# Kernel optimization log

Hardware: AMD Instinct MI355X
Metric: run time of the kernel (lower is better)

Reference implementation:

```python
import jax, jax.numpy as jnp
import numpy as np

B, S, E, H, WIN = 1, 2048, 1024, 16, 256
D = E // H  # head_out = 64


def setup_inputs() -> dict:
    key = jax.random.key(0)
    ks = jax.random.split(key, 10)
    w = lambda k: jax.random.normal(k, (E, E), jnp.float32) * 0.02
    return {
        'x': jax.random.normal(ks[0], (B, S, E), jnp.float32),
        'global_attention_mask': jax.random.randint(ks[1], (B, S), 0, 2).astype(jnp.int32),
        'W_local_query': w(ks[2]),
        'W_local_key': w(ks[3]),
        'W_local_value': w(ks[4]),
        'W_query': w(ks[5]),
        'W_key': w(ks[6]),
        'W_value': w(ks[7]),
        'W_proj': w(ks[8]),
        'b_proj': jnp.zeros((E,), jnp.float32),
    }


def reference(x, global_attention_mask, W_local_query, W_local_key, W_local_value,
              W_query, W_key, W_value, W_proj, b_proj):
    b, seq, emb = x.shape
    nH, dh, win = H, D, WIN
    chunks = seq // win
    NEG = -1e9
    scale = 1.0 / (dh ** 0.5)

    # ---- local (windowed) branch ----
    ql = x @ W_local_query            # [b,S,E]
    kl = x @ W_local_key
    vl = x @ W_local_value
    # NOTE: original does a direct .view -> plain reshape (no head transpose)
    qc = ql.reshape(b, nH, chunks, win, dh)
    kc = kl.reshape(b, nH, chunks, win, dh)
    vloc = vl.reshape(b, nH, seq, dh)
    s = jnp.einsum('bhcqd,bhckd->bhcqk', qc, kc)      # [b,H,C,W,W]
    causal_w = jnp.tril(jnp.ones((win, win), bool))
    s = jnp.where(causal_w, s, NEG) * scale           # mask then /sqrt(d), as in source
    s = s.mean(axis=2)                                # mean over chunks -> [b,H,W,W]
    s = jnp.pad(s, ((0, 0), (0, 0), (0, seq - win), (0, seq - win)))
    aw_l = jax.nn.softmax(s, axis=-1)                 # [b,H,S,S]
    local_ctx = jnp.einsum('bhqk,bhkd->bqhd', aw_l, vloc).reshape(b, seq, emb)

    # ---- global (full) branch ----
    q = (x @ W_query).reshape(b, seq, nH, dh).transpose(0, 2, 1, 3)
    k = (x @ W_key).reshape(b, seq, nH, dh).transpose(0, 2, 1, 3)
    v = (x @ W_value).reshape(b, seq, nH, dh).transpose(0, 2, 1, 3)
    sg = jnp.einsum('bhqd,bhkd->bhqk', q, k)          # [b,H,S,S]
    causal_s = jnp.tril(jnp.ones((seq, seq), bool))
    sg = jnp.where(causal_s, sg, NEG) * scale
    aw_g = jax.nn.softmax(sg, axis=-1)
    gctx = jnp.einsum('bhqk,bhkd->bqhd', aw_g, v).reshape(b, seq, emb)

    # ---- combine via global mask, then output projection ----
    ctx = jnp.where(global_attention_mask[:, :, None] == 1, gctx, local_ctx)
    return ctx @ W_proj + b_proj
```

## Files before the change

kernel.cpp:

```cpp
#include <hip/hip_runtime.h>
#include <hip/hip_bf16.h>

typedef _Float16 h8 __attribute__((ext_vector_type(8)));
typedef _Float16 h4 __attribute__((ext_vector_type(4)));
typedef _Float16 h2 __attribute__((ext_vector_type(2)));
typedef __fp16 fp16x2 __attribute__((ext_vector_type(2)));
typedef float f4 __attribute__((ext_vector_type(4)));

#define S_LEN 2048
#define EMB 1024
#define NH 16
#define DH 64

__device__ __forceinline__ void async_copy16(const void* g, void* l) {
  __builtin_amdgcn_global_load_lds(
      (const __attribute__((address_space(1))) void*)g,
      (__attribute__((address_space(3))) void*)l, 16, 0, 0);
}

__device__ __forceinline__ f4 mfma16(h8 a, h8 b, f4 c) {
  return __builtin_amdgcn_mfma_f32_16x16x32_f16(a, b, c, 0, 0, 0);
}

__device__ __forceinline__ h2 cvt_pk(float a, float b) {
  const fp16x2 r = __builtin_amdgcn_cvt_pkrtz(a, b);
  return __builtin_bit_cast(h2, r);
}

__global__ __launch_bounds__(256) void prep_kernel(
    const float* __restrict__ x, const float* w0, const float* w1, const float* w2,
    const float* w3, const float* w4, const float* w5, const float* w6,
    _Float16* __restrict__ xh, _Float16* __restrict__ Wtb) {
  const int bid = blockIdx.x;
  if (bid < 2048) {
    const int i = bid * 256 + threadIdx.x;
    const float4 v = *(const float4*)&x[(long)i * 4];
    h4 o;
    o.x = (_Float16)v.x; o.y = (_Float16)v.y; o.z = (_Float16)v.z; o.w = (_Float16)v.w;
    *(h4*)&xh[(long)i * 4] = o;
    return;
  }
  const int b2 = bid - 2048;
  const int z = b2 >> 10, rem = b2 & 1023;
  const float* W = w0;
  switch (z) {
    case 1: W = w1; break; case 2: W = w2; break; case 3: W = w3; break;
    case 4: W = w4; break; case 5: W = w5; break; case 6: W = w6; break;
    default: break;
  }
  __shared__ float t[32][33];
  const int bk = (rem & 31) * 32, bn = (rem >> 5) * 32;
  const int tx = threadIdx.x & 31, ty = threadIdx.x >> 5;
  #pragma unroll
  for (int i = 0; i < 4; ++i)
    t[ty + i * 8][tx] = W[(long)(bk + ty + i * 8) * 1024 + bn + tx];
  __syncthreads();
  _Float16* o = Wtb + (long)z * 1048576;
  #pragma unroll
  for (int i = 0; i < 4; ++i)
    o[(long)(bn + ty + i * 8) * 1024 + bk + tx] = (_Float16)t[tx][ty + i * 8];
}

__global__ __launch_bounds__(256) void shuffle_kernel(
    const _Float16* __restrict__ ql, const _Float16* __restrict__ kl,
    const _Float16* __restrict__ vl, const _Float16* __restrict__ vg,
    const int* __restrict__ gmask,
    _Float16* __restrict__ Aq, _Float16* __restrict__ Ak,
    _Float16* __restrict__ vgT, float* __restrict__ Vall, float* __restrict__ Vtail,
    int* __restrict__ qsel, int* __restrict__ qcnt) {
  const int bid = blockIdx.x;
  if (bid < 2048) {
    const _Float16* src = (bid >= 1024) ? kl : ql;
    _Float16* dst = (bid >= 1024) ? Ak : Aq;
    const int u = (bid & 1023) * 256 + threadIdx.x;
    const int dseg = u & 7, c = (u >> 3) & 7, q = (u >> 6) & 255, h = u >> 14;
    const long soff = (long)(h * 128 + c * 16 + (q >> 4)) * 1024 + (q & 15) * 64 + dseg * 8;
    *(h8*)&dst[(long)u * 8] = *(const h8*)&src[soff];
    return;
  }
  if (bid < 4096) {
    const int b2 = bid - 2048;
    __shared__ _Float16 t[32][33];
    const int bs = (b2 & 63) * 32, be = (b2 >> 6) * 32;
    const int tx = threadIdx.x & 31, ty = threadIdx.x >> 5;
    #pragma unroll
    for (int i = 0; i < 4; ++i)
      t[ty + i * 8][tx] = vg[(long)(bs + ty + i * 8) * 1024 + be + tx];
    __syncthreads();
    #pragma unroll
    for (int i = 0; i < 4; ++i)
      vgT[(long)(be + ty + i * 8) * 2048 + bs + tx] = t[tx][ty + i * 8];
    return;
  }
  if (bid < 4112) {
    const int hh = bid - 4096;
    const int d = threadIdx.x & 63, g = threadIdx.x >> 6;
    float sall = 0.f, shead = 0.f;
    for (int i = 0; i < 32; ++i) {
      const int ro = g * 32 + i;
      const _Float16* base = vl + (long)(hh * 128 + ro) * 1024 + d;
      #pragma unroll
      for (int j = 0; j < 16; ++j) {
        const float v = (float)base[j * 64];
        sall += v;
        if (ro < 16) shead += v;
      }
    }
    __shared__ float sA[4][64], sH[4][64];
    sA[g][d] = sall; sH[g][d] = shead;
    __syncthreads();
    if (g == 0) {
      const float a = sA[0][d] + sA[1][d] + sA[2][d] + sA[3][d];
      const float hsum = sH[0][d] + sH[1][d] + sH[2][d] + sH[3][d];
      Vall[hh * 64 + d] = a;
      Vtail[hh * 64 + d] = a - hsum;
    }
    return;
  }
  const int t = threadIdx.x;
  int m8[8], cnt8 = 0;
  #pragma unroll
  for (int j = 0; j < 8; ++j) {
    m8[j] = gmask[t * 8 + j];
    cnt8 += (m8[j] == 1);
  }
  __shared__ int sc[256];
  sc[t] = cnt8;
  __syncthreads();
  for (int off = 1; off < 256; off <<= 1) {
    const int v = (t >= off) ? sc[t - off] : 0;
    __syncthreads();
    sc[t] += v;
    __syncthreads();
  }
  int base = sc[t] - cnt8;
  #pragma unroll
  for (int j = 0; j < 8; ++j)
    if (m8[j] == 1) qsel[base++] = t * 8 + j;
  if (t == 255) qcnt[0] = sc[255];
}

__global__ __launch_bounds__(512, 2) void gemm256_kernel(
    const _Float16* __restrict__ A, const _Float16* __restrict__ Bt,
    _Float16* __restrict__ C) {
  const int bid = blockIdx.x;
  const int bxx = (bid >> 3) & 7;
  const int byy = (bid & 7) * 3 + (bid >> 6);
  const int bm = bxx * 256, bn = byy * 256;

  __shared__ alignas(16) _Float16 As[2][2][8192];
  __shared__ alignas(16) _Float16 Bs[2][2][8192];

  const int tid = threadIdx.x;
  const int w = tid >> 6, l = tid & 63;
  const int lo = l & 15, hi = l >> 4;
  const int wm = w >> 2, wn = w & 3;
  const int srow = tid >> 3;
  const int kseg = (tid & 7) ^ (srow & 7);

  const _Float16* Bb = Bt + (long)(byy >> 2) * 1048576 + (long)(bn & 1023) * 1024;

#define STG_A(db, half, tt) do {                                                     \
    const int t_ = (tt) < 15 ? (tt) : 15;                                            \
    const _Float16* s_ = A + (long)(bm + (half) * 128 + srow) * 1024 + t_ * 64 + kseg * 8; \
    async_copy16(s_, &As[db][half][w * 512]);                                        \
    async_copy16(s_ + 65536, &As[db][half][4096 + w * 512]);                         \
  } while (0)
#define STG_B(db, half, tt) do {                                                     \
    const int t_ = (tt) < 15 ? (tt) : 15;                                            \
    const _Float16* s_ = Bb + (long)((half) * 128 + srow) * 1024 + t_ * 64 + kseg * 8; \
    async_copy16(s_, &Bs[db][half][w * 512]);                                        \
    async_copy16(s_ + 65536, &Bs[db][half][4096 + w * 512]);                         \
  } while (0)
#define LDA(db, mg) do { _Pragma("unroll")                                           \
    for (int fr = 0; fr < 4; ++fr) {                                                 \
      const int rr = wm * 64 + fr * 16 + lo;                                         \
      _Pragma("unroll") for (int kk = 0; kk < 2; ++kk)                               \
        af[fr][kk] = *(const h8*)&As[db][mg][rr * 64 + (((kk * 4 + hi) ^ (rr & 7)) * 8)]; \
    } } while (0)
#define LDB(db, ng) do { _Pragma("unroll")                                           \
    for (int fc = 0; fc < 2; ++fc) {                                                 \
      const int rr = wn * 32 + fc * 16 + lo;                                         \
      _Pragma("unroll") for (int kk = 0; kk < 2; ++kk)                               \
        bf[ng][fc][kk] = *(const h8*)&Bs[db][ng][rr * 64 + (((kk * 4 + hi) ^ (rr & 7)) * 8)]; \
    } } while (0)
#define MFMA_PH(mg, ng) do {                                                         \
    __builtin_amdgcn_s_setprio(1);                                                   \
    _Pragma("unroll") for (int fr = 0; fr < 4; ++fr)                                 \
      _Pragma("unroll") for (int fc = 0; fc < 2; ++fc) {                             \
        acc[mg][fr][ng][fc] = mfma16(af[fr][0], bf[ng][fc][0], acc[mg][fr][ng][fc]); \
        acc[mg][fr][ng][fc] = mfma16(af[fr][1], bf[ng][fc][1], acc[mg][fr][ng][fc]); \
      }                                                                              \
    __builtin_amdgcn_s_setprio(0);                                                   \
  } while (0)
#define BARR do { asm volatile("" ::: "memory"); __builtin_amdgcn_s_barrier();       \
                  asm volatile("" ::: "memory"); } while (0)
#define VM8 asm volatile("s_waitcnt vmcnt(8)" ::: "memory")

  const f4 zero = {0.f, 0.f, 0.f, 0.f};
  f4 acc[2][4][2][2];
  #pragma unroll
  for (int a_ = 0; a_ < 2; ++a_)
    #pragma unroll
    for (int b_ = 0; b_ < 4; ++b_)
      #pragma unroll
      for (int c_ = 0; c_ < 2; ++c_)
        #pragma unroll
        for (int d_ = 0; d_ < 2; ++d_) acc[a_][b_][c_][d_] = zero;
  h8 af[4][2];
  h8 bf[2][2][2];

  STG_A(0, 0, 0); STG_B(0, 0, 0); STG_A(0, 1, 0); STG_B(0, 1, 0);
  STG_A(1, 0, 1); STG_B(1, 0, 1); STG_A(1, 1, 1);
  asm volatile("s_waitcnt vmcnt(6)" ::: "memory");
  BARR;

  for (int i = 0; i < 8; ++i) {
    const int t2 = 2 * i + 2, t3 = 2 * i + 3;
    LDA(0, 0); LDB(0, 0); STG_B(1, 1, 2 * i + 1); MFMA_PH(0, 0); VM8; BARR;
    LDB(0, 1); STG_A(0, 0, t2); MFMA_PH(0, 1); BARR;
    LDA(0, 1); STG_B(0, 0, t2); MFMA_PH(1, 0); BARR;
    STG_A(0, 1, t2); MFMA_PH(1, 1); VM8; BARR;
    LDA(1, 0); LDB(1, 0); STG_B(0, 1, t2); MFMA_PH(0, 0); VM8; BARR;
    LDB(1, 1); STG_A(1, 0, t3); MFMA_PH(0, 1); BARR;
    LDA(1, 1); STG_B(1, 0, t3); MFMA_PH(1, 0); BARR;
    STG_A(1, 1, t3); MFMA_PH(1, 1); VM8; BARR;
  }

  #pragma unroll
  for (int mg = 0; mg < 2; ++mg)
    #pragma unroll
    for (int fr = 0; fr < 4; ++fr) {
      const int row = bm + mg * 128 + wm * 64 + fr * 16 + hi * 4;
      #pragma unroll
      for (int ng = 0; ng < 2; ++ng)
        #pragma unroll
        for (int fc = 0; fc < 2; ++fc) {
          const int colg = bn + ng * 128 + wn * 32 + fc * 16 + lo;
          _Float16* cp = C + (long)(colg >> 10) * 2097152 + (long)row * 1024 + (colg & 1023);
          #pragma unroll
          for (int r = 0; r < 4; ++r)
            cp[(long)r * 1024] = (_Float16)acc[mg][fr][ng][fc][r];
        }
    }
#undef STG_A
#undef STG_B
#undef LDA
#undef LDB
#undef MFMA_PH
#undef BARR
#undef VM8
}

template <bool F32OUT, bool HAS_BIAS>
__global__ __launch_bounds__(256) void gemm_kernel(
    const _Float16* __restrict__ A, const _Float16* __restrict__ Bt,
    void* __restrict__ Cv, const float* __restrict__ bias,
    int M, int N, int K, long sA, long sB, long sC) {
  const int bxx = blockIdx.x, byy = blockIdx.y, bzz = blockIdx.z;
  const _Float16* Ab = A + (long)bzz * sA;
  const _Float16* Bb = Bt + (long)bzz * sB;
  const int bm = bxx * 128, bn = byy * 128;
  __shared__ alignas(16) _Float16 As[128 * 64];
  __shared__ alignas(16) _Float16 Bs[128 * 64];
  const int tid = threadIdx.x;
  const int w = tid >> 6, l = tid & 63;
  const int lo = l & 15, hi = l >> 4;
  const int wr = (w >> 1) * 64, wc = (w & 1) * 64;
  const int srow = l >> 3, ssp = l & 7;
  const int ssl = ssp ^ (srow & 7);

  const f4 zero = {0.f, 0.f, 0.f, 0.f};
  f4 acc[4][4];
  #pragma unroll
  for (int m = 0; m < 4; ++m)
    #pragma unroll
    for (int n = 0; n < 4; ++n) acc[m][n] = zero;

  for (int k0 = 0; k0 < K; k0 += 64) {
    #pragma unroll
    for (int i = 0; i < 4; ++i) {
      const int chunk = w + i * 4;
      async_copy16(&Ab[(long)(bm + chunk * 8 + srow) * K + k0 + ssl * 8], &As[chunk * 512]);
      async_copy16(&Bb[(long)(bn + chunk * 8 + srow) * K + k0 + ssl * 8], &Bs[chunk * 512]);
    }
    __syncthreads();
    #pragma unroll
    for (int kk = 0; kk < 2; ++kk) {
      h8 af[4], bff[4];
      #pragma unroll
      for (int m = 0; m < 4; ++m) {
        const int r = wr + m * 16 + lo;
        af[m] = *(const h8*)&As[r * 64 + (((kk * 4 + hi) ^ (r & 7)) * 8)];
      }
      #pragma unroll
      for (int n = 0; n < 4; ++n) {
        const int r = wc + n * 16 + lo;
        bff[n] = *(const h8*)&Bs[r * 64 + (((kk * 4 + hi) ^ (r & 7)) * 8)];
      }
      #pragma unroll
      for (int m = 0; m < 4; ++m)
        #pragma unroll
        for (int n = 0; n < 4; ++n)
          acc[m][n] = mfma16(af[m], bff[n], acc[m][n]);
    }
    __syncthreads();
  }

  #pragma unroll
  for (int m = 0; m < 4; ++m) {
    const int row0 = bm + wr + m * 16 + hi * 4;
    #pragma unroll
    for (int n = 0; n < 4; ++n) {
      const int col = bn + wc + n * 16 + lo;
      float bv = 0.f;
      if constexpr (HAS_BIAS) bv = bias[col];
      #pragma unroll
      for (int r = 0; r < 4; ++r) {
        const float v = acc[m][n][r] + bv;
        const long off = (long)bzz * sC + (long)(row0 + r) * N + col;
        if constexpr (F32OUT) ((float*)Cv)[off] = v;
        else ((_Float16*)Cv)[off] = (_Float16)v;
      }
    }
  }
}

__global__ __launch_bounds__(256) void gemm64_kernel(
    const _Float16* __restrict__ A, const _Float16* __restrict__ Bt,
    float* __restrict__ C, const float* __restrict__ bias, int N, int K) {
  const int bm = blockIdx.x * 64, bn = blockIdx.y * 128;
  __shared__ alignas(16) _Float16 As[64 * 64];
  __shared__ alignas(16) _Float16 Bs[128 * 64];
  const int tid = threadIdx.x;
  const int w = tid >> 6, l = tid & 63;
  const int lo = l & 15, hi = l >> 4;
  const int wc = w * 32;
  const int srow = l >> 3, ssp = l & 7;
  const int ssl = ssp ^ (srow & 7);

  const f4 zero = {0.f, 0.f, 0.f, 0.f};
  f4 acc[4][2];
  #pragma unroll
  for (int m = 0; m < 4; ++m)
    #pragma unroll
    for (int n = 0; n < 2; ++n) acc[m][n] = zero;

  for (int k0 = 0; k0 < K; k0 += 64) {
    #pragma unroll
    for (int i = 0; i < 6; ++i) {
      const int c = w + i * 4;
      if (c < 8)
        async_copy16(&A[(long)(bm + c * 8 + srow) * K + k0 + ssl * 8], &As[c * 512]);
      else
        async_copy16(&Bt[(long)(bn + (c - 8) * 8 + srow) * K + k0 + ssl * 8], &Bs[(c - 8) * 512]);
    }
    __syncthreads();
    #pragma unroll
    for (int kk = 0; kk < 2; ++kk) {
      h8 af[4], bff[2];
      #pragma unroll
      for (int m = 0; m < 4; ++m) {
        const int r = m * 16 + lo;
        af[m] = *(const h8*)&As[r * 64 + (((kk * 4 + hi) ^ (r & 7)) * 8)];
      }
      #pragma unroll
      for (int n = 0; n < 2; ++n) {
        const int r = wc + n * 16 + lo;
        bff[n] = *(const h8*)&Bs[r * 64 + (((kk * 4 + hi) ^ (r & 7)) * 8)];
      }
      #pragma unroll
      for (int m = 0; m < 4; ++m)
        #pragma unroll
        for (int n = 0; n < 2; ++n)
          acc[m][n] = mfma16(af[m], bff[n], acc[m][n]);
    }
    __syncthreads();
  }

  #pragma unroll
  for (int m = 0; m < 4; ++m) {
    const int row0 = bm + m * 16 + hi * 4;
    #pragma unroll
    for (int n = 0; n < 2; ++n) {
      const int col = bn + wc + n * 16 + lo;
      const float bv = bias ? bias[col] : 0.f;
      #pragma unroll
      for (int r = 0; r < 4; ++r)
        C[(long)(row0 + r) * N + col] = acc[m][n][r] + bv;
    }
  }
}

__global__ __launch_bounds__(256) void flash_kernel(
    const _Float16* __restrict__ Q, const _Float16* __restrict__ Km,
    const _Float16* __restrict__ Vt, const int* __restrict__ qsel,
    const int* __restrict__ qcnt, _Float16* __restrict__ ctx,
    _Float16* __restrict__ pO, float2* __restrict__ ml) {
  const int bx = blockIdx.x;
  const int h = bx & 15;
  const int v = bx >> 4;
  const int tile = 31 - (v >> 1);
  const int chunk = v & 1;
  int cnt = qcnt[0];
  cnt = cnt < 1 ? 1 : (cnt > 2048 ? 2048 : cnt);
  if (tile * 64 >= cnt) return;
  const int L = (qsel[min(tile * 64 + 63, cnt - 1)] & 2047) + 1;
  const int ntot = (L + 63) >> 6;
  const bool chunked = (ntot > 16);
  if (!chunked && chunk) return;
  const int nsplit = chunked ? ((ntot + 1) >> 1) : ntot;
  const int t0 = chunk ? nsplit : 0;
  const int t1 = chunk ? ntot : nsplit;

  const int tid = threadIdx.x;
  const int w = tid >> 6, l = tid & 63;
  const int lo = l & 15, hi = l >> 4;
  const int row = tile * 64 + w * 16 + lo;
  const int qg = qsel[min(row, cnt - 1)] & 2047;

  __shared__ alignas(16) _Float16 Ks[2][64 * 64];
  __shared__ alignas(16) _Float16 Vs[2][64 * 64];
  __shared__ alignas(16) _Float16 Ps[4][16 * 80];
  _Float16* ps = Ps[w];

  const int rl = tid >> 3;
  const int ssl = (tid & 7) ^ (rl & 7);

#define STAGE(b, t)                                                                   \
  do {                                                                                \
    async_copy16(&Km[(long)((t) * 64 + rl) * EMB + h * DH + ssl * 8],                 \
                 &Ks[(b)][(w * 8) * 64]);                                             \
    async_copy16(&Km[(long)((t) * 64 + 32 + rl) * EMB + h * DH + ssl * 8],            \
                 &Ks[(b)][(w * 8 + 32) * 64]);                                        \
    async_copy16(&Vt[(long)(h * DH + rl) * S_LEN + (t) * 64 + ssl * 8],               \
                 &Vs[(b)][(w * 8) * 64]);                                             \
    async_copy16(&Vt[(long)(h * DH + 32 + rl) * S_LEN + (t) * 64 + ssl * 8],          \
                 &Vs[(b)][(w * 8 + 32) * 64]);                                        \
  } while (0)

  h8 qf[2];
  #pragma unroll
  for (int kk = 0; kk < 2; ++kk)
    qf[kk] = *(const h8*)&Q[(long)qg * EMB + h * DH + kk * 32 + hi * 8];

  const f4 zero = {0.f, 0.f, 0.f, 0.f};
  f4 o[4];
  #pragma unroll
  for (int nd = 0; nd < 4; ++nd) o[nd] = zero;
  float mr = -1e30f, lr = 0.f;
  const float SC = 0.125f * 1.44269504f;

  STAGE(0, t0);
  __syncthreads();
  int cur = 0;

  for (int t = t0; t < t1; ++t) {
    if (t + 1 < t1) STAGE(cur ^ 1, t + 1);

    const _Float16* ks = Ks[cur];
    const _Float16* vs = Vs[cur];

    __builtin_amdgcn_s_setprio(1);
    f4 s[4];
    #pragma unroll
    for (int n = 0; n < 4; ++n) {
      s[n] = zero;
      #pragma unroll
      for (int kk = 0; kk < 2; ++kk) {
        const int r = n * 16 + lo;
        const h8 kf = *(const h8*)&ks[r * 64 + (((kk * 4 + hi) ^ (lo & 7)) * 8)];
        s[n] = mfma16(kf, qf[kk], s[n]);
      }
    }
    __builtin_amdgcn_s_setprio(0);

    float sv[16];
    float tm = -1e30f;
    #pragma unroll
    for (int n = 0; n < 4; ++n)
      #pragma unroll
      for (int r = 0; r < 4; ++r) {
        float vv = s[n][r] * SC;
        if ((t * 64 + n * 16 + hi * 4 + r) > qg) vv = -1e30f;
        sv[n * 4 + r] = vv;
        tm = fmaxf(tm, vv);
      }
    tm = fmaxf(tm, __shfl_xor(tm, 16));
    tm = fmaxf(tm, __shfl_xor(tm, 32));
    const float mn = fmaxf(mr, tm);
    const float c = exp2f(mr - mn);
    mr = mn;
    float psum = 0.f;
    #pragma unroll
    for (int i = 0; i < 16; ++i) {
      sv[i] = exp2f(sv[i] - mr);
      psum += sv[i];
    }
    psum += __shfl_xor(psum, 16);
    psum += __shfl_xor(psum, 32);
    lr = lr * c + psum;

    #pragma unroll
    for (int n = 0; n < 4; ++n) {
      const int seg = (2 * n + (hi >> 1)) ^ (lo & 7);
      const int base = lo * 80 + seg * 8 + (hi & 1) * 4;
      *(h2*)&ps[base] = cvt_pk(sv[n * 4 + 0], sv[n * 4 + 1]);
      *(h2*)&ps[base + 2] = cvt_pk(sv[n * 4 + 2], sv[n * 4 + 3]);
    }
    h8 pb[2];
    #pragma unroll
    for (int kk = 0; kk < 2; ++kk)
      pb[kk] = *(const h8*)&ps[lo * 80 + (((kk * 4 + hi) ^ (lo & 7)) * 8)];

    __builtin_amdgcn_s_setprio(1);
    #pragma unroll
    for (int nd = 0; nd < 4; ++nd) {
      #pragma unroll
      for (int r = 0; r < 4; ++r) o[nd][r] *= c;
      #pragma unroll
      for (int kk = 0; kk < 2; ++kk) {
        const int rr = nd * 16 + lo;
        const h8 vf = *(const h8*)&vs[rr * 64 + (((kk * 4 + hi) ^ (lo & 7)) * 8)];
        o[nd] = mfma16(vf, pb[kk], o[nd]);
      }
    }
    __builtin_amdgcn_s_setprio(0);

    __syncthreads();
    cur ^= 1;
  }
#undef STAGE

  if (chunked) {
    const int slot = (h * 32 + tile) * 2 + chunk;
    _Float16* po = pO + (long)slot * 4096 + (w * 16 + lo) * 64;
    #pragma unroll
    for (int nd = 0; nd < 4; ++nd) {
      const h2 a = cvt_pk(o[nd][0], o[nd][1]);
      const h2 b = cvt_pk(o[nd][2], o[nd][3]);
      const h4 v4 = {a[0], a[1], b[0], b[1]};
      *(h4*)&po[nd * 16 + hi * 4] = v4;
    }
    if (hi == 0) ml[slot * 64 + w * 16 + lo] = make_float2(mr, lr);
  } else if (row < cnt) {
    const float inv = 1.f / lr;
    #pragma unroll
    for (int nd = 0; nd < 4; ++nd) {
      const h2 a = cvt_pk(o[nd][0] * inv, o[nd][1] * inv);
      const h2 b = cvt_pk(o[nd][2] * inv, o[nd][3] * inv);
      const h4 v4 = {a[0], a[1], b[0], b[1]};
      *(h4*)&ctx[(long)qg * EMB + h * DH + nd * 16 + hi * 4] = v4;
    }
  }
}

__global__ __launch_bounds__(256) void localfin_kernel(
    const _Float16* __restrict__ P, const _Float16* __restrict__ vl,
    const float* __restrict__ Vall, const float* __restrict__ Vtail,
    const _Float16* __restrict__ pO, const float2* __restrict__ ml,
    const int* __restrict__ gmask, const int* __restrict__ qsel,
    const int* __restrict__ qcnt, _Float16* __restrict__ ctx) {
  const int bid = blockIdx.x;
  const int tid = threadIdx.x;
  if (bid < 1024) {
    const int q = bid & 255, hg = bid >> 8;
    if (gmask[q] == 1) return;
    const int sub = tid >> 6, l = tid & 63;
    const int hh = hg * 4 + sub;
    __shared__ float wgt[4][256];
    const _Float16* Pr = P + ((long)hh * 256 + q) * 256;
    float sv[4];
    bool valid[4];
    float M = -1e30f;
    #pragma unroll
    for (int i = 0; i < 4; ++i) {
      const int k = l + i * 64;
      valid[i] = (k <= q);
      sv[i] = valid[i] ? (float)Pr[k] * 0.015625f : -1e30f;
      M = fmaxf(M, sv[i]);
    }
    M = fmaxf(M, __shfl_xor(M, 1));
    M = fmaxf(M, __shfl_xor(M, 2));
    M = fmaxf(M, __shfl_xor(M, 4));
    M = fmaxf(M, __shfl_xor(M, 8));
    M = fmaxf(M, __shfl_xor(M, 16));
    M = fmaxf(M, __shfl_xor(M, 32));
    M = fmaxf(M, 0.f);
    float ps = 0.f;
    #pragma unroll
    for (int i = 0; i < 4; ++i) {
      const float e = valid[i] ? __expf(sv[i] - M) : 0.f;
      wgt[sub][l + i * 64] = e;
      ps += e;
    }
    ps += __shfl_xor(ps, 1);
    ps += __shfl_xor(ps, 2);
    ps += __shfl_xor(ps, 4);
    ps += __shfl_xor(ps, 8);
    ps += __shfl_xor(ps, 16);
    ps += __shfl_xor(ps, 32);
    const float em = __expf(-M);
    const float denom = ps + 1792.f * em;
    const int d = l;
    float acc = em * Vtail[hh * 64 + d];
    const _Float16* vb = vl + (long)hh * 128 * 1024 + d;
    for (int k = 0; k <= q; ++k)
      acc += wgt[sub][k] * (float)vb[(long)(k >> 4) * 1024 + (k & 15) * 64];
    ctx[(long)q * EMB + hh * DH + d] = (_Float16)(acc / denom);
    return;
  }
  if (bid < 8192) {
    const int gid = (bid - 1024) * 256 + tid;
    const int s = 256 + (gid >> 10), e = gid & 1023;
    if (gmask[s] == 0)
      ctx[(long)s * EMB + e] = (_Float16)(Vall[e] * (1.f / 2048.f));
    return;
  }
  const int b2 = bid - 8192;
  const int h = b2 & 15, tile = b2 >> 4;
  int cnt = qcnt[0];
  cnt = cnt < 1 ? 1 : (cnt > 2048 ? 2048 : cnt);
  if (tile * 64 >= cnt) return;
  const int L = (qsel[min(tile * 64 + 63, cnt - 1)] & 2047) + 1;
  if (((L + 63) >> 6) <= 16) return;
  const int q = tid >> 2, ds = (tid & 3) * 16;
  const int row = tile * 64 + q;
  if (row >= cnt) return;
  const int sg = qsel[row] & 2047;
  const int slot0 = (h * 32 + tile) * 2, slot1 = slot0 + 1;
  const float2 ml0 = ml[slot0 * 64 + q];
  const float2 ml1 = ml[slot1 * 64 + q];
  const float M = fmaxf(ml0.x, ml1.x);
  const float w0 = exp2f(ml0.x - M), w1 = exp2f(ml1.x - M);
  const float inv = 1.f / (w0 * ml0.y + w1 * ml1.y);
  const h8 a0 = *(const h8*)&pO[(long)slot0 * 4096 + q * 64 + ds];
  const h8 a1 = *(const h8*)&pO[(long)slot0 * 4096 + q * 64 + ds + 8];
  const h8 b0 = *(const h8*)&pO[(long)slot1 * 4096 + q * 64 + ds];
  const h8 b1 = *(const h8*)&pO[(long)slot1 * 4096 + q * 64 + ds + 8];
  h8 r0, r1;
  #pragma unroll
  for (int j = 0; j < 8; ++j) {
    r0[j] = (_Float16)((w0 * (float)a0[j] + w1 * (float)b0[j]) * inv);
    r1[j] = (_Float16)((w0 * (float)a1[j] + w1 * (float)b1[j]) * inv);
  }
  *(h8*)&ctx[(long)sg * EMB + h * DH + ds] = r0;
  *(h8*)&ctx[(long)sg * EMB + h * DH + ds + 8] = r1;
}

extern "C" void kernel_launch(void* const* d_in, const int* in_sizes, int n_in,
                              void* d_out, int out_size, void* d_ws, size_t ws_size,
                              hipStream_t stream) {
  const float* x = (const float*)d_in[0];
  const int* gmask = (const int*)d_in[1];
  const float* Wlq = (const float*)d_in[2];
  const float* Wlk = (const float*)d_in[3];
  const float* Wlv = (const float*)d_in[4];
  const float* Wq = (const float*)d_in[5];
  const float* Wk = (const float*)d_in[6];
  const float* Wv = (const float*)d_in[7];
  const float* Wp = (const float*)d_in[8];
  const float* bp = (const float*)d_in[9];
  float* out = (float*)d_out;

  char* ws = (char*)d_ws;
  _Float16* xh = (_Float16*)(ws);
  _Float16* Wtb = (_Float16*)(ws + (4u << 20));
  _Float16* proj = (_Float16*)(ws + (18u << 20));
  _Float16* ql = proj;
  _Float16* kl = (_Float16*)(ws + (22u << 20));
  _Float16* vl = (_Float16*)(ws + (26u << 20));
  _Float16* qg = (_Float16*)(ws + (30u << 20));
  _Float16* kg = (_Float16*)(ws + (34u << 20));
  _Float16* vg = (_Float16*)(ws + (38u << 20));
  _Float16* Aq = (_Float16*)(ws + (4u << 20));
  _Float16* Ak = (_Float16*)(ws + (8u << 20));
  _Float16* P = (_Float16*)(ws + (12u << 20));
  float* Vall = (float*)(ws + (14u << 20));
  float* Vtail = (float*)(ws + (14u << 20) + 4096);
  float2* ml = (float2*)(ws + (14u << 20) + 16384);
  int* qsel = (int*)(ws + (14u << 20) + 614400);
  int* qcnt = (int*)(ws + (14u << 20) + 622592);
  _Float16* Wpt = (_Float16*)(ws + (16u << 20));
  _Float16* vgT = (_Float16*)(ws);
  _Float16* ctx = (_Float16*)(ws + (18u << 20));
  _Float16* pO = (_Float16*)(ws + (4u << 20));

  prep_kernel<<<9216, 256, 0, stream>>>(x, Wlq, Wlk, Wlv, Wq, Wk, Wv, Wp, xh, Wtb);
  gemm256_kernel<<<192, 512, 0, stream>>>(xh, Wtb, proj);
  shuffle_kernel<<<4113, 256, 0, stream>>>(ql, kl, vl, vg, gmask, Aq, Ak, vgT,
                                           Vall, Vtail, qsel, qcnt);
  gemm_kernel<false, false><<<dim3(2, 2, 16), 256, 0, stream>>>(
      Aq, Ak, P, nullptr, 256, 256, 512, 131072L, 131072L, 65536L);
  flash_kernel<<<1024, 256, 0, stream>>>(qg, kg, vgT, qsel, qcnt, ctx, pO, ml);
  localfin_kernel<<<8704, 256, 0, stream>>>(P, vl, Vall, Vtail, pO, ml, gmask,
                                            qsel, qcnt, ctx);
  gemm64_kernel<<<dim3(32, 8), 256, 0, stream>>>(ctx, Wpt, out, bp, 1024, 1024);
}
```

Baseline: 140.1 us.

## Fuse local-score GEMM and mean-fill into flash kernel; double-buffer output projection GEMM

Folds the small batched local-score GEMM and the constant mean-fill of non-global context rows into extra blocks of the flash attention launch, using a shared raw smem buffer. This removes a kernel launch and lets that work overlap with attention, and the fill now uses vectorised 8-wide stores. The output projection GEMM moves to 64x64 tiles with double-buffered async LDS staging, giving more blocks and overlapping loads with MFMA. pO is relocated in the workspace so it no longer aliases Aq, which is now read concurrently.

Result: faster. 123.8 us (-11.7%).

```diff
diff --git a/kernel.cpp b/kernel.cpp
--- a/kernel.cpp
+++ b/kernel.cpp
@@ -252,143 +252,61 @@
 #undef VM8
 }
 
-template <bool F32OUT, bool HAS_BIAS>
-__global__ __launch_bounds__(256) void gemm_kernel(
+__global__ __launch_bounds__(256) void gemm64_kernel(
     const _Float16* __restrict__ A, const _Float16* __restrict__ Bt,
-    void* __restrict__ Cv, const float* __restrict__ bias,
-    int M, int N, int K, long sA, long sB, long sC) {
-  const int bxx = blockIdx.x, byy = blockIdx.y, bzz = blockIdx.z;
-  const _Float16* Ab = A + (long)bzz * sA;
-  const _Float16* Bb = Bt + (long)bzz * sB;
-  const int bm = bxx * 128, bn = byy * 128;
-  __shared__ alignas(16) _Float16 As[128 * 64];
-  __shared__ alignas(16) _Float16 Bs[128 * 64];
+    float* __restrict__ C, const float* __restrict__ bias) {
+  const int bm = blockIdx.x * 64, bn = blockIdx.y * 64;
+  __shared__ alignas(16) _Float16 As[2][4096];
+  __shared__ alignas(16) _Float16 Bs[2][4096];
   const int tid = threadIdx.x;
   const int w = tid >> 6, l = tid & 63;
   const int lo = l & 15, hi = l >> 4;
-  const int wr = (w >> 1) * 64, wc = (w & 1) * 64;
-  const int srow = l >> 3, ssp = l & 7;
-  const int ssl = ssp ^ (srow & 7);
+  const int srow = tid >> 3;
+  const int ssl = (tid & 7) ^ (srow & 7);
+
+#define STG64(b, k0) do {                                                            \
+    async_copy16(&A[(long)(bm + srow) * 1024 + (k0) + ssl * 8], &As[b][(w * 8) * 64]); \
+    async_copy16(&A[(long)(bm + 32 + srow) * 1024 + (k0) + ssl * 8],                 \
+                 &As[b][(w * 8 + 32) * 64]);                                         \
+    async_copy16(&Bt[(long)(bn + srow) * 1024 + (k0) + ssl * 8], &Bs[b][(w * 8) * 64]); \
+    async_copy16(&Bt[(long)(bn + 32 + srow) * 1024 + (k0) + ssl * 8],                \
+                 &Bs[b][(w * 8 + 32) * 64]);                                         \
+  } while (0)
 
   const f4 zero = {0.f, 0.f, 0.f, 0.f};
-  f4 acc[4][4];
-  #pragma unroll
-  for (int m = 0; m < 4; ++m)
-    #pragma unroll
-    for (int n = 0; n < 4; ++n) acc[m][n] = zero;
-
-  for (int k0 = 0; k0 < K; k0 += 64) {
-    #pragma unroll
-    for (int i = 0; i < 4; ++i) {
-      const int chunk = w + i * 4;
-      async_copy16(&Ab[(long)(bm + chunk * 8 + srow) * K + k0 + ssl * 8], &As[chunk * 512]);
-      async_copy16(&Bb[(long)(bn + chunk * 8 + srow) * K + k0 + ssl * 8], &Bs[chunk * 512]);
+  f4 acc[4];
+  #pragma unroll
+  for (int n = 0; n < 4; ++n) acc[n] = zero;
+
+  STG64(0, 0);
+  __syncthreads();
+  int cur = 0;
+  for (int k0 = 0; k0 < 1024; k0 += 64) {
+    if (k0 + 64 < 1024) STG64(cur ^ 1, k0 + 64);
+    #pragma unroll
+    for (int kk = 0; kk < 2; ++kk) {
+      const int ra = w * 16 + lo;
+      const h8 af = *(const h8*)&As[cur][ra * 64 + (((kk * 4 + hi) ^ (ra & 7)) * 8)];
+      #pragma unroll
+      for (int n = 0; n < 4; ++n) {
+        const int rb = n * 16 + lo;
+        const h8 bff = *(const h8*)&Bs[cur][rb * 64 + (((kk * 4 + hi) ^ (rb & 7)) * 8)];
+        acc[n] = mfma16(af, bff, acc[n]);
+      }
     }
     __syncthreads();
-    #pragma unroll
-    for (int kk = 0; kk < 2; ++kk) {
-      h8 af[4], bff[4];
-      #pragma unroll
-      for (int m = 0; m < 4; ++m) {
-        const int r = wr + m * 16 + lo;
-        af[m] = *(const h8*)&As[r * 64 + (((kk * 4 + hi) ^ (r & 7)) * 8)];
-      }
-      #pragma unroll
-      for (int n = 0; n < 4; ++n) {
-        const int r = wc + n * 16 + lo;
-        bff[n] = *(const h8*)&Bs[r * 64 + (((kk * 4 + hi) ^ (r & 7)) * 8)];
-      }
-      #pragma unroll
-      for (int m = 0; m < 4; ++m)
-        #pragma unroll
-        for (int n = 0; n < 4; ++n)
-          acc[m][n] = mfma16(af[m], bff[n], acc[m][n]);
-    }
-    __syncthreads();
-  }
-
-  #pragma unroll
-  for (int m = 0; m < 4; ++m) {
-    const int row0 = bm + wr + m * 16 + hi * 4;
-    #pragma unroll
-    for (int n = 0; n < 4; ++n) {
-      const int col = bn + wc + n * 16 + lo;
-      float bv = 0.f;
-      if constexpr (HAS_BIAS) bv = bias[col];
-      #pragma unroll
-      for (int r = 0; r < 4; ++r) {
-        const float v = acc[m][n][r] + bv;
-        const long off = (long)bzz * sC + (long)(row0 + r) * N + col;
-        if constexpr (F32OUT) ((float*)Cv)[off] = v;
-        else ((_Float16*)Cv)[off] = (_Float16)v;
-      }
-    }
-  }
-}
-
-__global__ __launch_bounds__(256) void gemm64_kernel(
-    const _Float16* __restrict__ A, const _Float16* __restrict__ Bt,
-    float* __restrict__ C, const float* __restrict__ bias, int N, int K) {
-  const int bm = blockIdx.x * 64, bn = blockIdx.y * 128;
-  __shared__ alignas(16) _Float16 As[64 * 64];
-  __shared__ alignas(16) _Float16 Bs[128 * 64];
-  const int tid = threadIdx.x;
-  const int w = tid >> 6, l = tid & 63;
-  const int lo = l & 15, hi = l >> 4;
-  const int wc = w * 32;
-  const int srow = l >> 3, ssp = l & 7;
-  const int ssl = ssp ^ (srow & 7);
-
-  const f4 zero = {0.f, 0.f, 0.f, 0.f};
-  f4 acc[4][2];
-  #pragma unroll
-  for (int m = 0; m < 4; ++m)
-    #pragma unroll
-    for (int n = 0; n < 2; ++n) acc[m][n] = zero;
-
-  for (int k0 = 0; k0 < K; k0 += 64) {
-    #pragma unroll
-    for (int i = 0; i < 6; ++i) {
-      const int c = w + i * 4;
-      if (c < 8)
-        async_copy16(&A[(long)(bm + c * 8 + srow) * K + k0 + ssl * 8], &As[c * 512]);
-      else
-        async_copy16(&Bt[(long)(bn + (c - 8) * 8 + srow) * K + k0 + ssl * 8], &Bs[(c - 8) * 512]);
-    }
-    __syncthreads();
-    #pragma unroll
-    for (int kk = 0; kk < 2; ++kk) {
-      h8 af[4], bff[2];
-      #pragma unroll
-      for (int m = 0; m < 4; ++m) {
-        const int r = m * 16 + lo;
-        af[m] = *(const h8*)&As[r * 64 + (((kk * 4 + hi) ^ (r & 7)) * 8)];
-      }
-      #pragma unroll
-      for (int n = 0; n < 2; ++n) {
-        const int r = wc + n * 16 + lo;
-        bff[n] = *(const h8*)&Bs[r * 64 + (((kk * 4 + hi) ^ (r & 7)) * 8)];
-      }
-      #pragma unroll
-      for (int m = 0; m < 4; ++m)
-        #pragma unroll
-        for (int n = 0; n < 2; ++n)
-          acc[m][n] = mfma16(af[m], bff[n], acc[m][n]);
-    }
-    __syncthreads();
-  }
-
-  #pragma unroll
-  for (int m = 0; m < 4; ++m) {
-    const int row0 = bm + m * 16 + hi * 4;
-    #pragma unroll
-    for (int n = 0; n < 2; ++n) {
-      const int col = bn + wc + n * 16 + lo;
-      const float bv = bias ? bias[col] : 0.f;
-      #pragma unroll
-      for (int r = 0; r < 4; ++r)
-        C[(long)(row0 + r) * N + col] = acc[m][n][r] + bv;
-    }
+    cur ^= 1;
+  }
+#undef STG64
+
+  #pragma unroll
+  for (int n = 0; n < 4; ++n) {
+    const int col = bn + n * 16 + lo;
+    const float bv = bias[col];
+    const int row0 = bm + w * 16 + hi * 4;
+    #pragma unroll
+    for (int r = 0; r < 4; ++r)
+      C[(long)(row0 + r) * 1024 + col] = acc[n][r] + bv;
   }
 }
 
@@ -396,8 +314,91 @@
     const _Float16* __restrict__ Q, const _Float16* __restrict__ Km,
     const _Float16* __restrict__ Vt, const int* __restrict__ qsel,
     const int* __restrict__ qcnt, _Float16* __restrict__ ctx,
-    _Float16* __restrict__ pO, float2* __restrict__ ml) {
+    _Float16* __restrict__ pO, float2* __restrict__ ml,
+    const _Float16* __restrict__ Aq, const _Float16* __restrict__ Ak,
+    _Float16* __restrict__ P, const float* __restrict__ Vall,
+    const int* __restrict__ gmask) {
+  __shared__ alignas(16) char smem[43008];
   const int bx = blockIdx.x;
+  const int tid = threadIdx.x;
+
+  if (bx >= 1088) {
+    const int gid = (bx - 1088) * 256 + tid;
+    const int s = 256 + (gid >> 7), e8 = (gid & 127) * 8;
+    if (gmask[s] == 0) {
+      h8 v;
+      #pragma unroll
+      for (int j = 0; j < 8; ++j)
+        v[j] = (_Float16)(Vall[e8 + j] * (1.f / 2048.f));
+      *(h8*)&ctx[(long)s * EMB + e8] = v;
+    }
+    return;
+  }
+
+  if (bx >= 1024) {
+    const int b = bx - 1024;
+    const int bzz = b >> 2, bxx = (b >> 1) & 1, byy = b & 1;
+    const _Float16* Ab = Aq + (long)bzz * 131072;
+    const _Float16* Bb = Ak + (long)bzz * 131072;
+    const int bm = bxx * 128, bn = byy * 128;
+    _Float16* As = (_Float16*)smem;
+    _Float16* Bs = (_Float16*)(smem + 16384);
+    const int w = tid >> 6, l = tid & 63;
+    const int lo = l & 15, hi = l >> 4;
+    const int wr = (w >> 1) * 64, wc = (w & 1) * 64;
+    const int srow = l >> 3, ssp = l & 7;
+    const int ssl = ssp ^ (srow & 7);
+
+    const f4 zero = {0.f, 0.f, 0.f, 0.f};
+    f4 acc[4][4];
+    #pragma unroll
+    for (int m = 0; m < 4; ++m)
+      #pragma unroll
+      for (int n = 0; n < 4; ++n) acc[m][n] = zero;
+
+    for (int k0 = 0; k0 < 512; k0 += 64) {
+      #pragma unroll
+      for (int i = 0; i < 4; ++i) {
+        const int chunk = w + i * 4;
+        async_copy16(&Ab[(long)(bm + chunk * 8 + srow) * 512 + k0 + ssl * 8], &As[chunk * 512]);
+        async_copy16(&Bb[(long)(bn + chunk * 8 + srow) * 512 + k0 + ssl * 8], &Bs[chunk * 512]);
+      }
+      __syncthreads();
+      #pragma unroll
+      for (int kk = 0; kk < 2; ++kk) {
+        h8 af[4], bff[4];
+        #pragma unroll
+        for (int m = 0; m < 4; ++m) {
+          const int r = wr + m * 16 + lo;
+          af[m] = *(const h8*)&As[r * 64 + (((kk * 4 + hi) ^ (r & 7)) * 8)];
+        }
+        #pragma unroll
+        for (int n = 0; n < 4; ++n) {
+          const int r = wc + n * 16 + lo;
+          bff[n] = *(const h8*)&Bs[r * 64 + (((kk * 4 + hi) ^ (r & 7)) * 8)];
+        }
+        #pragma unroll
+        for (int m = 0; m < 4; ++m)
+          #pragma unroll
+          for (int n = 0; n < 4; ++n)
+            acc[m][n] = mfma16(af[m], bff[n], acc[m][n]);
+      }
+      __syncthreads();
+    }
+    #pragma unroll
+    for (int m = 0; m < 4; ++m) {
+      const int row0 = bm + wr + m * 16 + hi * 4;
+      #pragma unroll
+      for (int n = 0; n < 4; ++n) {
+        const int col = bn + wc + n * 16 + lo;
+        #pragma unroll
+        for (int r = 0; r < 4; ++r)
+          P[(long)bzz * 65536 + (long)(row0 + r) * 256 + col] = (_Float16)acc[m][n][r];
+      }
+    }
+    return;
+  }
+
   const int h = bx & 15;
   const int v = bx >> 4;
   const int tile = 31 - (v >> 1);
@@ -413,16 +414,14 @@
   const int t0 = chunk ? nsplit : 0;
   const int t1 = chunk ? ntot : nsplit;
 
-  const int tid = threadIdx.x;
   const int w = tid >> 6, l = tid & 63;
   const int lo = l & 15, hi = l >> 4;
   const int row = tile * 64 + w * 16 + lo;
   const int qg = qsel[min(row, cnt - 1)] & 2047;
 
-  __shared__ alignas(16) _Float16 Ks[2][64 * 64];
-  __shared__ alignas(16) _Float16 Vs[2][64 * 64];
-  __shared__ alignas(16) _Float16 Ps[4][16 * 80];
-  _Float16* ps = Ps[w];
+  _Float16* KsB = (_Float16*)smem;
+  _Float16* VsB = (_Float16*)(smem + 16384);
+  _Float16* ps = (_Float16*)(smem + 32768) + w * 1280;
 
   const int rl = tid >> 3;
   const int ssl = (tid & 7) ^ (rl & 7);
@@ -430,13 +429,13 @@
 #define STAGE(b, t)                                                                   \
   do {                                                                                \
     async_copy16(&Km[(long)((t) * 64 + rl) * EMB + h * DH + ssl * 8],                 \
-                 &Ks[(b)][(w * 8) * 64]);                                             \
+                 &KsB[(b) * 4096 + (w * 8) * 64]);                                    \
     async_copy16(&Km[(long)((t) * 64 + 32 + rl) * EMB + h * DH + ssl * 8],            \
-                 &Ks[(b)][(w * 8 + 32) * 64]);                                        \
+                 &KsB[(b) * 4096 + (w * 8 + 32) * 64]);                               \
     async_copy16(&Vt[(long)(h * DH + rl) * S_LEN + (t) * 64 + ssl * 8],               \
-                 &Vs[(b)][(w * 8) * 64]);                                             \
+                 &VsB[(b) * 4096 + (w * 8) * 64]);                                    \
     async_copy16(&Vt[(long)(h * DH + 32 + rl) * S_LEN + (t) * 64 + ssl * 8],          \
-                 &Vs[(b)][(w * 8 + 32) * 64]);                                        \
+                 &VsB[(b) * 4096 + (w * 8 + 32) * 64]);                               \
   } while (0)
 
   h8 qf[2];
@@ -458,8 +457,8 @@
   for (int t = t0; t < t1; ++t) {
     if (t + 1 < t1) STAGE(cur ^ 1, t + 1);
 
-    const _Float16* ks = Ks[cur];
-    const _Float16* vs = Vs[cur];
+    const _Float16* ks = KsB + cur * 4096;
+    const _Float16* vs = VsB + cur * 4096;
 
     __builtin_amdgcn_s_setprio(1);
     f4 s[4];
@@ -557,7 +556,7 @@
 
 __global__ __launch_bounds__(256) void localfin_kernel(
     const _Float16* __restrict__ P, const _Float16* __restrict__ vl,
-    const float* __restrict__ Vall, const float* __restrict__ Vtail,
+    const float* __restrict__ Vtail,
     const _Float16* __restrict__ pO, const float2* __restrict__ ml,
     const int* __restrict__ gmask, const int* __restrict__ qsel,
     const int* __restrict__ qcnt, _Float16* __restrict__ ctx) {
@@ -610,14 +609,7 @@
     ctx[(long)q * EMB + hh * DH + d] = (_Float16)(acc / denom);
     return;
   }
-  if (bid < 8192) {
-    const int gid = (bid - 1024) * 256 + tid;
-    const int s = 256 + (gid >> 10), e = gid & 1023;
-    if (gmask[s] == 0)
-      ctx[(long)s * EMB + e] = (_Float16)(Vall[e] * (1.f / 2048.f));
-    return;
-  }
-  const int b2 = bid - 8192;
+  const int b2 = bid - 1024;
   const int h = b2 & 15, tile = b2 >> 4;
   int cnt = qcnt[0];
   cnt = cnt < 1 ? 1 : (cnt > 2048 ? 2048 : cnt);
@@ -684,16 +676,15 @@
   _Float16* Wpt = (_Float16*)(ws + (16u << 20));
   _Float16* vgT = (_Float16*)(ws);
   _Float16* ctx = (_Float16*)(ws + (18u << 20));
-  _Float16* pO = (_Float16*)(ws + (4u << 20));
+  _Float16* pO = (_Float16*)(ws + (38u << 20));
 
   prep_kernel<<<9216, 256, 0, stream>>>(x, Wlq, Wlk, Wlv, Wq, Wk, Wv, Wp, xh, Wtb);
   gemm256_kernel<<<192, 512, 0, stream>>>(xh, Wtb, proj);
   shuffle_kernel<<<4113, 256, 0, stream>>>(ql, kl, vl, vg, gmask, Aq, Ak, vgT,
                                            Vall, Vtail, qsel, qcnt);
-  gemm_kernel<false, false><<<dim3(2, 2, 16), 256, 0, stream>>>(
-      Aq, Ak, P, nullptr, 256, 256, 512, 131072L, 131072L, 65536L);
-  flash_kernel<<<1024, 256, 0, stream>>>(qg, kg, vgT, qsel, qcnt, ctx, pO, ml);
-  localfin_kernel<<<8704, 256, 0, stream>>>(P, vl, Vall, Vtail, pO, ml, gmask,
+  flash_kernel<<<1984, 256, 0, stream>>>(qg, kg, vgT, qsel, qcnt, ctx, pO, ml,
+                                         Aq, Ak, P, Vall, gmask);
+  localfin_kernel<<<1536, 256, 0, stream>>>(P, vl, Vtail, pO, ml, gmask,
                                             qsel, qcnt, ctx);
-  gemm64_kernel<<<dim3(32, 8), 256, 0, stream>>>(ctx, Wpt, out, bp, 1024, 1024);
-}
+  gemm64_kernel<<<dim3(32, 16), 256, 0, stream>>>(ctx, Wpt, out, bp);
+}
```
